# Kernel optimization log

Hardware: AMD Instinct MI355X
Metric: run time of the kernel (lower is better)

The kernel has to match this reference:

```python
import jax, jax.numpy as jnp
import numpy as np

B, S, D, H = 4096, 200, 128, 64


def setup_inputs() -> dict:
    key = jax.random.key(0)
    ks = jax.random.split(key, 8)
    X_series = jax.random.normal(ks[0], (B, S, D), dtype=jnp.float32)
    pos_series = jax.random.normal(ks[1], (S, D), dtype=jnp.float32)
    X_item = jax.random.normal(ks[2], (B, D), dtype=jnp.float32)
    valid_mask = jax.random.randint(ks[3], (B, S), 0, 2) > 0
    valid_mask = valid_mask.at[:, 0].set(True)  # avoid all-masked rows (NaN softmax)
    glorot = jax.nn.initializers.glorot_uniform()
    Wc = glorot(ks[4], (D, H), jnp.float32)
    Wp = glorot(ks[5], (D, H), jnp.float32)
    We = glorot(ks[6], (D, H), jnp.float32)
    z = jax.random.normal(ks[7], (H,), dtype=jnp.float32) * 0.1
    return {"X_series": X_series, "pos_series": pos_series, "X_item": X_item,
            "valid_mask": valid_mask, "Wc": Wc, "Wp": Wp, "We": We, "z": z}


def reference(X_series, pos_series, X_item, valid_mask, Wc, Wp, We, z):
    # additive attention pre-activation: [B,S,H]
    pre = (X_item @ Wc)[:, None, :] + X_series @ We + (pos_series @ Wp)[None, :, :]
    # scores: sum over hidden of z * tanh(pre) -> [B,S]
    scores = jnp.einsum('bsh,h->bs', jnp.tanh(pre), z)
    # raw masked score sum (pre-softmax), [B,1]
    score_sum = jnp.sum(jnp.where(valid_mask, scores, 0.0), axis=-1, keepdims=True)
    # masked softmax over seq
    attn = jax.nn.softmax(jnp.where(valid_mask, scores, -jnp.inf), axis=-1)
    # weighted sum over seq -> [B,D]
    attention_output = jnp.einsum('bs,bsd->bd', attn, X_series)
    return jnp.concatenate([attention_output, score_sum], axis=1)
```

## Files before the change

kernel.cpp:

```cpp
#include <hip/hip_runtime.h>

#define BB 4096
#define SS 200
#define DD 128
#define HH 64
#define NT 13
#define OUTW (DD + 1)

typedef __attribute__((ext_vector_type(4))) float f32x4;
typedef _Float16 f16x8 __attribute__((ext_vector_type(8)));

template <int CTRL>
__device__ __forceinline__ float dpp_add(float x) {
  int xi = __float_as_int(x);
  int yi = __builtin_amdgcn_update_dpp(xi, xi, CTRL, 0xF, 0xF, false);
  return x + __int_as_float(yi);
}
__device__ __forceinline__ float row16_sum(float x) {
  x = dpp_add<0xB1>(x);
  x = dpp_add<0x4E>(x);
  x = dpp_add<0x124>(x);
  x = dpp_add<0x128>(x);
  return x;
}

__global__ void setupA_kernel(const float* __restrict__ pos,
                              const float* __restrict__ Wp,
                              const float* __restrict__ We,
                              const void* __restrict__ maskv,
                              _Float16* __restrict__ Bfrag,
                              _Float16* __restrict__ Psw,
                              int* __restrict__ flag) {
  __shared__ int anyf[4];
  const int blk = blockIdx.x;
  const int t = threadIdx.x;
  if (blk < NT) {
    const int tile = blk;
    for (int id = t; id < 1024; id += 256) {
      const int half = id >> 9;
      const int lane = (id >> 3) & 63;
      const int e = id & 7;
      const int ct = (half << 1) | (e >> 2);
      const int r = e & 3;
      int s = tile * 16 + ((lane >> 4) << 2) + r;
      if (s >= SS) s = SS - 1;
      const int h = ct * 16 + (lane & 15);
      const float* pr = pos + (size_t)s * DD;
      const float* wp = Wp + h;
      float a0 = 0.f, a1 = 0.f;
      #pragma unroll 8
      for (int d = 0; d < DD; d += 2) {
        a0 = fmaf(pr[d], wp[d * HH], a0);
        a1 = fmaf(pr[d + 1], wp[(d + 1) * HH], a1);
      }
      Psw[((size_t)(tile * 2 + half) * 64 + lane) * 8 + e] = (_Float16)(a0 + a1);
    }
  } else if (blk == NT) {
    for (int id = t; id < 1024; id += 256) {
      int lane = id & 63;
      int kt = (id >> 6) & 3;
      int ct = id >> 8;
      int kbase = kt * 32 + 8 * (lane >> 4);
      int n = ct * 16 + (lane & 15);
      _Float16* dst = Bfrag + id * 8;
      #pragma unroll
      for (int j = 0; j < 8; ++j) dst[j] = (_Float16)We[(kbase + j) * HH + n];
    }
  } else {
    const unsigned char* mb = (const unsigned char*)maskv;
    int local = 0;
    for (int i = t; i < 4096; i += 256)
      if ((i & 3) != 0 && mb[i] != 0) local = 1;
    unsigned long long bal = __ballot(local != 0);
    if ((t & 63) == 0) anyf[t >> 6] = (bal != 0ull) ? 1 : 0;
    __syncthreads();
    if (t == 0) *flag = (anyf[0] | anyf[1] | anyf[2] | anyf[3]);
  }
}

__global__ void setupB_kernel(const float* __restrict__ Xi,
                              const float* __restrict__ Wc,
                              const void* __restrict__ maskv,
                              const int* __restrict__ flagp,
                              float* __restrict__ cw,
                              unsigned short* __restrict__ mbitsArr) {
  const int t = threadIdx.x;
  const int w = t >> 6, lane = t & 63;
  const int base = blockIdx.x * 8;
  {
    const int b0 = base + w * 2;
    const float* xi0 = Xi + (size_t)b0 * DD;
    const float* xi1 = xi0 + DD;
    const float* wc = Wc + lane;
    float a0 = 0.f, a1 = 0.f;
    #pragma unroll 8
    for (int d = 0; d < DD; ++d) {
      const float wv = wc[d * HH];
      a0 = fmaf(xi0[d], wv, a0);
      a1 = fmaf(xi1[d], wv, a1);
    }
    cw[(size_t)b0 * HH + lane] = a0;
    cw[(size_t)(b0 + 1) * HH + lane] = a1;
  }
  if (t < 128) {
    const int b = base + (t >> 4);
    const int lr = t & 15;
    const int mflag = *flagp;
    unsigned mb = 0;
    if (mflag) {
      const unsigned char* mbp = (const unsigned char*)maskv + (size_t)b * SS;
      #pragma unroll
      for (int tt = 0; tt < NT; ++tt) {
        const int srow = tt * 16 + lr;
        unsigned v = (srow < SS) ? (unsigned)mbp[srow] : 0u;
        mb |= (v ? 1u : 0u) << tt;
      }
    } else {
      const int* mip = (const int*)maskv + (size_t)b * SS;
      #pragma unroll
      for (int tt = 0; tt < NT; ++tt) {
        const int srow = tt * 16 + lr;
        unsigned v = (srow < SS) ? (unsigned)(mip[srow] != 0) : 0u;
        mb |= v << tt;
      }
    }
    mbitsArr[(size_t)b * 16 + lr] = (unsigned short)mb;
  }
}

__global__ __launch_bounds__(256, 2) void fused_kernel(
    const float* __restrict__ Xs,
    const float* __restrict__ zv, const float* __restrict__ cw,
    const unsigned short* __restrict__ mbitsArr,
    const _Float16* __restrict__ Comb,
    float* __restrict__ out) {
  __shared__ __align__(16) float xlds[4][2][2048];

  const int t = threadIdx.x;
  const int lane = t & 63;
  const int w = t >> 6;
  const int lg = lane >> 4;
  const int lr = lane & 15;
  const int b = blockIdx.x * 4 + w;

  const float* Xrow = Xs + (size_t)b * (SS * DD);
  const f16x8* pswb = (const f16x8*)(Comb + 8192);

  auto stage_tile = [&](int tt, int buf) {
    float* dst = &xlds[w][buf][0];
    #pragma unroll
    for (int k = 0; k < 8; ++k) {
      const int row = 2 * k + (lane >> 5);
      int grow = tt * 16 + row; if (grow >= SS) grow = SS - 1;
      const int c = (lane & 31) ^ row;
      const float* src = Xrow + (size_t)grow * DD + c * 4;
      __builtin_amdgcn_global_load_lds(
          (const __attribute__((address_space(1))) void*)src,
          (__attribute__((address_space(3))) void*)(dst + k * 256),
          16, 0, 0);
    }
  };

  stage_tile(0, 0);
  f16x8 pn0 = pswb[lane];
  f16x8 pn1 = pswb[64 + lane];

  f16x8 bfr[16];
  {
    const f16x8* bg = (const f16x8*)Comb;
    #pragma unroll
    for (int i = 0; i < 16; ++i) bfr[i] = bg[i * 64 + lane];
  }

  float c4[4], z4[4];
  #pragma unroll
  for (int ct = 0; ct < 4; ++ct) {
    c4[ct] = cw[(size_t)b * HH + ct * 16 + lr];
    z4[ct] = zv[ct * 16 + lr];
  }
  const unsigned mbits = mbitsArr[(size_t)b * 16 + lr];

  float part[4][8];
  #pragma unroll
  for (int kt = 0; kt < 4; ++kt)
    #pragma unroll
    for (int j = 0; j < 8; ++j) part[kt][j] = 0.f;
  float usum = 0.f, ssum = 0.f;
  int cur = 0;

  for (int tt = 0; tt < NT; ++tt) {
    asm volatile("s_waitcnt vmcnt(0)" ::: "memory");
    __builtin_amdgcn_sched_barrier(0);
    f32x4 acc[4];
    #pragma unroll
    for (int ct = 0; ct < 4; ++ct) {
      #pragma unroll
      for (int r = 0; r < 4; ++r) {
        const float pv = (ct < 2) ? (float)pn0[ct * 4 + r] : (float)pn1[(ct - 2) * 4 + r];
        acc[ct][r] = pv + c4[ct];
      }
    }
    if (tt + 1 < NT) {
      stage_tile(tt + 1, cur ^ 1);
      pn0 = pswb[(tt + 1) * 128 + lane];
      pn1 = pswb[(tt + 1) * 128 + 64 + lane];
    }
    const float* bufp = &xlds[w][cur][0];
    f16x8 af[4];
    #pragma unroll
    for (int kt = 0; kt < 4; ++kt) {
      const int ch = lg * 2 + kt * 8;
      const f32x4 v0 = *(const f32x4*)&bufp[lr * 128 + (((ch    ) ^ lr) * 4)];
      const f32x4 v1 = *(const f32x4*)&bufp[lr * 128 + (((ch + 1) ^ lr) * 4)];
      f16x8 v;
      v[0] = (_Float16)v0[0]; v[1] = (_Float16)v0[1];
      v[2] = (_Float16)v0[2]; v[3] = (_Float16)v0[3];
      v[4] = (_Float16)v1[0]; v[5] = (_Float16)v1[1];
      v[6] = (_Float16)v1[2]; v[7] = (_Float16)v1[3];
      af[kt] = v;
    }
    #pragma unroll
    for (int kt = 0; kt < 4; ++kt)
      #pragma unroll
      for (int ct = 0; ct < 4; ++ct)
        acc[ct] = __builtin_amdgcn_mfma_f32_16x16x32_f16(af[kt], bfr[ct * 4 + kt], acc[ct], 0, 0, 0);
    float sc[4];
    #pragma unroll
    for (int r = 0; r < 4; ++r) {
      float p = 0.f;
      #pragma unroll
      for (int ct = 0; ct < 4; ++ct) {
        const float e2 = __expf(2.f * acc[ct][r]);
        const float th = 1.f - 2.f * __builtin_amdgcn_rcpf(e2 + 1.f);
        p = fmaf(z4[ct], th, p);
      }
      sc[r] = row16_sum(p);
    }
    const float s01 = (lr & 1) ? sc[1] : sc[0];
    const float s23 = (lr & 1) ? sc[3] : sc[2];
    const float sel = (lr & 2) ? s23 : s01;
    const float mysc = __shfl(sel, ((lr >> 2) << 4) | lr, 64);
    const bool mv = (mbits >> tt) & 1u;
    const float u = mv ? __expf(mysc) : 0.f;
    ssum += mv ? mysc : 0.f;
    usum += u;
    #pragma unroll
    for (int kt = 0; kt < 4; ++kt)
      #pragma unroll
      for (int j = 0; j < 8; ++j)
        part[kt][j] = fmaf(u, (float)af[kt][j], part[kt][j]);
    cur ^= 1;
  }

  #pragma unroll
  for (int kt = 0; kt < 4; ++kt)
    #pragma unroll
    for (int j = 0; j < 8; ++j)
      part[kt][j] = row16_sum(part[kt][j]);
  usum = row16_sum(usum);
  ssum = row16_sum(ssum);

  const float inv = 1.f / usum;
  if (lr == 0) {
    float* ob = out + (size_t)b * OUTW;
    #pragma unroll
    for (int kt = 0; kt < 4; ++kt)
      #pragma unroll
      for (int j = 0; j < 8; ++j)
        ob[kt * 32 + lg * 8 + j] = part[kt][j] * inv;
  }
  if (lane == 8) out[(size_t)b * OUTW + DD] = ssum;
}

extern "C" void kernel_launch(void* const* d_in, const int* in_sizes, int n_in,
                              void* d_out, int out_size, void* d_ws, size_t ws_size,
                              hipStream_t stream) {
  const float* Xs  = (const float*)d_in[0];
  const float* pos = (const float*)d_in[1];
  const float* Xi  = (const float*)d_in[2];
  const void*  mk  = d_in[3];
  const float* Wc  = (const float*)d_in[4];
  const float* Wp  = (const float*)d_in[5];
  const float* We  = (const float*)d_in[6];
  const float* zv  = (const float*)d_in[7];
  float* out = (float*)d_out;

  char* ws = (char*)d_ws;
  int*            flag  = (int*)ws;
  _Float16*       Bfrag = (_Float16*)(ws + 256);
  _Float16*       Psw   = (_Float16*)(ws + 256 + 16384);
  float*          cw    = (float*)(ws + 43520);
  unsigned short* mbA   = (unsigned short*)(ws + 43520 + (size_t)BB * HH * 4);

  setupA_kernel<<<NT + 2, 256, 0, stream>>>(pos, Wp, We, mk, Bfrag, Psw, flag);
  setupB_kernel<<<BB / 8, 256, 0, stream>>>(Xi, Wc, mk, flag, cw, mbA);
  fused_kernel<<<BB / 4, 256, 0, stream>>>(Xs, zv, cw, mbA, Bfrag, out);
}
```

Baseline: 113.9 us.

## Spread pos@Wp setup across more blocks and rebalance setup kernels

The pos@Wp projection moves out of 13 serial blocks, where each thread computed 4 redundant dot products, into 200 blocks with one row each, written to an fp32 intermediate. The fragment swizzle and mask-bit packing move into a second setup kernel, and the Xi@Wc projection moves into the first. This removes the long serial tail of the small setupA launch, at the cost of an extra intermediate buffer round-trip and a repartitioned workspace layout.

```diff
diff --git a/kernel.cpp b/kernel.cpp
--- a/kernel.cpp
+++ b/kernel.cpp
@@ -24,14 +24,69 @@
   return x;
 }
 
-__global__ void setupA_kernel(const float* __restrict__ pos,
-                              const float* __restrict__ Wp,
-                              const float* __restrict__ We,
+__global__ void setup_kernel(const float* __restrict__ pos,
+                             const float* __restrict__ Wp,
+                             const float* __restrict__ We,
+                             const void* __restrict__ maskv,
+                             const float* __restrict__ Xi,
+                             const float* __restrict__ Wc,
+                             float* __restrict__ Pmat,
+                             _Float16* __restrict__ Bfrag,
+                             float* __restrict__ cw,
+                             int* __restrict__ flag) {
+  __shared__ int anyf[4];
+  const int blk = blockIdx.x;
+  const int t = threadIdx.x;
+  if (blk < SS) {
+    if (t < HH) {
+      float acc = 0.f;
+      #pragma unroll 8
+      for (int d = 0; d < DD; ++d) acc = fmaf(pos[blk * DD + d], Wp[d * HH + t], acc);
+      Pmat[blk * HH + t] = acc;
+    }
+  } else if (blk == SS) {
+    for (int id = t; id < 1024; id += 256) {
+      int lane = id & 63;
+      int kt = (id >> 6) & 3;
+      int ct = id >> 8;
+      int kbase = kt * 32 + 8 * (lane >> 4);
+      int n = ct * 16 + (lane & 15);
+      _Float16* dst = Bfrag + id * 8;
+      #pragma unroll
+      for (int j = 0; j < 8; ++j) dst[j] = (_Float16)We[(kbase + j) * HH + n];
+    }
+  } else if (blk == SS + 1) {
+    const unsigned char* mb = (const unsigned char*)maskv;
+    int local = 0;
+    for (int i = t; i < 4096; i += 256)
+      if ((i & 3) != 0 && mb[i] != 0) local = 1;
+    unsigned long long bal = __ballot(local != 0);
+    if ((t & 63) == 0) anyf[t >> 6] = (bal != 0ull) ? 1 : 0;
+    __syncthreads();
+    if (t == 0) *flag = (anyf[0] | anyf[1] | anyf[2] | anyf[3]);
+  } else {
+    const int w = t >> 6, lane = t & 63;
+    const int base = (blk - (SS + 2)) * 8 + w * 2;
+    const float* xi0 = Xi + (size_t)base * DD;
+    const float* xi1 = xi0 + DD;
+    const float* wc = Wc + lane;
+    float a0 = 0.f, a1 = 0.f;
+    #pragma unroll 8
+    for (int d = 0; d < DD; ++d) {
+      const float wv = wc[d * HH];
+      a0 = fmaf(xi0[d], wv, a0);
+      a1 = fmaf(xi1[d], wv, a1);
+    }
+    cw[(size_t)base * HH + lane] = a0;
+    cw[(size_t)(base + 1) * HH + lane] = a1;
+  }
+}
+
+__global__ void setup2_kernel(const float* __restrict__ Pmat,
                               const void* __restrict__ maskv,
-                              _Float16* __restrict__ Bfrag,
+                              const int* __restrict__ flagp,
                               _Float16* __restrict__ Psw,
-                              int* __restrict__ flag) {
-  __shared__ int anyf[4];
+                              unsigned short* __restrict__ mbitsArr) {
   const int blk = blockIdx.x;
   const int t = threadIdx.x;
   if (blk < NT) {
@@ -44,87 +99,35 @@
       const int r = e & 3;
       int s = tile * 16 + ((lane >> 4) << 2) + r;
       if (s >= SS) s = SS - 1;
-      const int h = ct * 16 + (lane & 15);
-      const float* pr = pos + (size_t)s * DD;
-      const float* wp = Wp + h;
-      float a0 = 0.f, a1 = 0.f;
-      #pragma unroll 8
-      for (int d = 0; d < DD; d += 2) {
-        a0 = fmaf(pr[d], wp[d * HH], a0);
-        a1 = fmaf(pr[d + 1], wp[(d + 1) * HH], a1);
+      Psw[((size_t)(tile * 2 + half) * 64 + lane) * 8 + e] =
+          (_Float16)Pmat[s * HH + ct * 16 + (lane & 15)];
+    }
+  } else {
+    const int base = (blk - NT) * 8;
+    if (t < 128) {
+      const int b = base + (t >> 4);
+      const int lr = t & 15;
+      const int mflag = *flagp;
+      unsigned mb = 0;
+      if (mflag) {
+        const unsigned char* mbp = (const unsigned char*)maskv + (size_t)b * SS;
+        #pragma unroll
+        for (int tt = 0; tt < NT; ++tt) {
+          const int srow = tt * 16 + lr;
+          unsigned v = (srow < SS) ? (unsigned)mbp[srow] : 0u;
+          mb |= (v ? 1u : 0u) << tt;
+        }
+      } else {
+        const int* mip = (const int*)maskv + (size_t)b * SS;
+        #pragma unroll
+        for (int tt = 0; tt < NT; ++tt) {
+          const int srow = tt * 16 + lr;
+          unsigned v = (srow < SS) ? (unsigned)(mip[srow] != 0) : 0u;
+          mb |= v << tt;
+        }
       }
-      Psw[((size_t)(tile * 2 + half) * 64 + lane) * 8 + e] = (_Float16)(a0 + a1);
-    }
-  } else if (blk == NT) {
-    for (int id = t; id < 1024; id += 256) {
-      int lane = id & 63;
-      int kt = (id >> 6) & 3;
-      int ct = id >> 8;
-      int kbase = kt * 32 + 8 * (lane >> 4);
-      int n = ct * 16 + (lane & 15);
-      _Float16* dst = Bfrag + id * 8;
-      #pragma unroll
-      for (int j = 0; j < 8; ++j) dst[j] = (_Float16)We[(kbase + j) * HH + n];
-    }
-  } else {
-    const unsigned char* mb = (const unsigned char*)maskv;
-    int local = 0;
-    for (int i = t; i < 4096; i += 256)
-      if ((i & 3) != 0 && mb[i] != 0) local = 1;
-    unsigned long long bal = __ballot(local != 0);
-    if ((t & 63) == 0) anyf[t >> 6] = (bal != 0ull) ? 1 : 0;
-    __syncthreads();
-    if (t == 0) *flag = (anyf[0] | anyf[1] | anyf[2] | anyf[3]);
-  }
-}
-
-__global__ void setupB_kernel(const float* __restrict__ Xi,
-                              const float* __restrict__ Wc,
-                              const void* __restrict__ maskv,
-                              const int* __restrict__ flagp,
-                              float* __restrict__ cw,
-                              unsigned short* __restrict__ mbitsArr) {
-  const int t = threadIdx.x;
-  const int w = t >> 6, lane = t & 63;
-  const int base = blockIdx.x * 8;
-  {
-    const int b0 = base + w * 2;
-    const float* xi0 = Xi + (size_t)b0 * DD;
-    const float* xi1 = xi0 + DD;
-    const float* wc = Wc + lane;
-    float a0 = 0.f, a1 = 0.f;
-    #pragma unroll 8
-    for (int d = 0; d < DD; ++d) {
-      const float wv = wc[d * HH];
-      a0 = fmaf(xi0[d], wv, a0);
-      a1 = fmaf(xi1[d], wv, a1);
-    }
-    cw[(size_t)b0 * HH + lane] = a0;
-    cw[(size_t)(b0 + 1) * HH + lane] = a1;
-  }
-  if (t < 128) {
-    const int b = base + (t >> 4);
-    const int lr = t & 15;
-    const int mflag = *flagp;
-    unsigned mb = 0;
-    if (mflag) {
-      const unsigned char* mbp = (const unsigned char*)maskv + (size_t)b * SS;
-      #pragma unroll
-      for (int tt = 0; tt < NT; ++tt) {
-        const int srow = tt * 16 + lr;
-        unsigned v = (srow < SS) ? (unsigned)mbp[srow] : 0u;
-        mb |= (v ? 1u : 0u) << tt;
-      }
-    } else {
-      const int* mip = (const int*)maskv + (size_t)b * SS;
-      #pragma unroll
-      for (int tt = 0; tt < NT; ++tt) {
-        const int srow = tt * 16 + lr;
-        unsigned v = (srow < SS) ? (unsigned)(mip[srow] != 0) : 0u;
-        mb |= v << tt;
-      }
-    }
-    mbitsArr[(size_t)b * 16 + lr] = (unsigned short)mb;
+      mbitsArr[(size_t)b * 16 + lr] = (unsigned short)mb;
+    }
   }
 }
 
@@ -287,12 +290,14 @@
 
   char* ws = (char*)d_ws;
   int*            flag  = (int*)ws;
-  _Float16*       Bfrag = (_Float16*)(ws + 256);
-  _Float16*       Psw   = (_Float16*)(ws + 256 + 16384);
-  float*          cw    = (float*)(ws + 43520);
-  unsigned short* mbA   = (unsigned short*)(ws + 43520 + (size_t)BB * HH * 4);
-
-  setupA_kernel<<<NT + 2, 256, 0, stream>>>(pos, Wp, We, mk, Bfrag, Psw, flag);
-  setupB_kernel<<<BB / 8, 256, 0, stream>>>(Xi, Wc, mk, flag, cw, mbA);
+  float*          Pmat  = (float*)(ws + 256);
+  _Float16*       Bfrag = (_Float16*)(ws + 256 + SS * HH * 4);
+  _Float16*       Psw   = (_Float16*)(ws + 67840);
+  float*          cw    = (float*)(ws + 94464);
+  unsigned short* mbA   = (unsigned short*)(ws + 94464 + (size_t)BB * HH * 4);
+
+  setup_kernel<<<SS + 2 + BB / 8, 256, 0, stream>>>(pos, Wp, We, mk, Xi, Wc,
+                                                    Pmat, Bfrag, cw, flag);
+  setup2_kernel<<<NT + BB / 8, 256, 0, stream>>>(Pmat, mk, flag, Psw, mbA);
   fused_kernel<<<BB / 4, 256, 0, stream>>>(Xs, zv, cw, mbA, Bfrag, out);
 }
```

Result: faster. 95.33 us (-16.3%).
